# Kernel optimization log

Hardware: AMD Instinct MI355X
Metric: run time of the kernel (lower is better)

## Reference

```python
import jax, jax.numpy as jnp
import numpy as np

DT = 1e-3  # integration timestep (init kwarg dt)


def setup_inputs() -> dict:
    key = jax.random.key(0)
    ks = jax.random.split(key, 10)
    B, T, S, H = 4096, 2048, 1, 64
    # physically sensible signals: v ~ N(0,1), 0 < F_c < F_s so g > 0
    v = jax.random.normal(ks[0], (B, T, S), dtype=jnp.float32)
    F_c = 0.5 + jax.random.uniform(ks[1], (B, T, S), dtype=jnp.float32)
    F_s = F_c + 0.5 + 0.5 * jax.random.uniform(ks[2], (B, T, S), dtype=jnp.float32)
    x = jnp.concatenate([v, F_c, F_s], axis=-1)  # [B, T, 3*S]
    u01 = lambda k, shp: jax.random.uniform(k, shp, minval=0.0, maxval=0.1, dtype=jnp.float32)
    return {
        "x": x,
        "sigma_1": u01(ks[3], (1, S)),
        "sigma_2": u01(ks[4], (1, S)),
        "alpha": u01(ks[5], (1, S)),
        "v_s": u01(ks[6], (1, S)),
        "W1": jax.random.normal(ks[7], (2 * S, H), dtype=jnp.float32) * 0.1,
        "b1": jnp.zeros((H,), jnp.float32),
        "W2": jax.random.normal(ks[8], (H, S), dtype=jnp.float32) * 0.1,
        "b2": jnp.zeros((S,), jnp.float32),
    }


def reference(x, sigma_1, sigma_2, alpha, v_s, W1, b1, W2, b2):
    """LuGreCell.callv3 unrolled over time via lax.scan. x: [B,T,3S] -> F: [B,T,S]."""
    s1 = jnp.abs(sigma_1)
    s2 = jnp.abs(sigma_2)

    def step(sz0, xt):  # sz0: [B,S], xt: [B,3S]
        v, F_c, F_s = jnp.split(xt, 3, axis=-1)
        # sigma_call: MLP on concat([v, sz_0])
        mi = jnp.concatenate([v, sz0], axis=-1)  # [B, 2S]
        sigma_0 = jax.nn.softplus(jnp.tanh(mi @ W1 + b1) @ W2 + b2)  # [B, S]
        g = F_c + (F_s - F_c) * jnp.exp(-jnp.abs(v / v_s) ** alpha)
        k = g * jnp.sign(v)
        sz = k + (sz0 - k) * jnp.exp(-DT * sigma_0 * jnp.abs(v) / g)
        zdot = v - sz * jnp.abs(v) / g  # uses pre-clip sz, as in original
        sz = jnp.clip(sz, -F_s, F_s)
        F = sz + s1 * zdot + s2 * v
        return sz, F

    B = x.shape[0]
    S = x.shape[-1] // 3
    xT = jnp.swapaxes(x, 0, 1)  # [T, B, 3S]
    sz_init = jnp.zeros((B, S), x.dtype)
    _, F_seq = jax.lax.scan(step, sz_init, xT)  # F_seq: [T, B, S]
    return jnp.swapaxes(F_seq, 0, 1)  # [B, T, S]
```

## Files before the change

### kernel.cpp

```cpp
#include <hip/hip_runtime.h>


#define DT 1e-3f
#define NV 256
#define VMINF (-6.6f)
#define VMAXF (6.6f)
#define ZAF   (2.56f)

__global__ __launch_bounds__(320) void coef_kernel(
    const float* __restrict__ W1,
    const float* __restrict__ b1,
    const float* __restrict__ W2,
    const float* __restrict__ b2,
    float4* __restrict__ tabA,
    float*  __restrict__ tabB)
{
    __shared__ float fsh[5];
    const int iv = blockIdx.x;
    const int j  = threadIdx.x >> 6;
    const int h  = threadIdx.x & 63;
    const float v = VMINF + iv * ((VMAXF - VMINF) / (NV - 1));
    const float pn = 0.95105651629f * ZAF;
    const float qn = 0.58778525229f * ZAF;
    const float szv = (j == 0) ? pn : (j == 1) ? -pn
                    : (j == 2) ? qn : (j == 3) ? -qn : 0.f;
    const float pre = fmaf(v, W1[h], fmaf(szv, W1[64 + h], b1[h]));
    float c = W2[h] * tanhf(pre);
#pragma unroll
    for (int o = 32; o; o >>= 1) c += __shfl_down(c, o);
    if (h == 0) {
        const float y = c + b2[0];
        fsh[j] = fmaxf(y, 0.f) + log1pf(expf(-fabsf(y)));
    }
    __syncthreads();
    if (threadIdx.x == 0) {
        const float f0 = fsh[0], f1 = fsh[1], f2 = fsh[2], f3 = fsh[3];
        const float c0 = fsh[4];
        const float P = pn * pn, Q = qn * qn;
        const float ep = 0.5f * (f0 + f1) - c0;
        const float eq = 0.5f * (f2 + f3) - c0;
        const float op = 0.5f * (f0 - f1);
        const float oq = 0.5f * (f2 - f3);
        const float invPQ = 1.f / (P - Q);
        const float c4 = (ep / P - eq / Q) * invPQ;
        const float c2 = ep / P - c4 * P;
        const float c3 = (op / pn - oq / qn) * invPQ;
        const float c1 = op / pn - c3 * P;
        tabA[iv] = make_float4(-DT * c0, -DT * c1, -DT * c2, -DT * c3);
        tabB[iv] = -DT * c4;
    }
}

template <int L>
__device__ __forceinline__ float rb(float v) {
    const int s = __float_as_int(v);
    return __int_as_float(
        __builtin_amdgcn_update_dpp(s, s, 0x150 | L, 0xf, 0xf, false));
}

__global__ __launch_bounds__(256, 1) void lugre_kernel(
    const float* __restrict__ x,
    const float* __restrict__ sigma1,
    const float* __restrict__ sigma2,
    const float* __restrict__ alpha_p,
    const float* __restrict__ vs_p,
    const float4* __restrict__ tabA,
    const float*  __restrict__ tabB,
    float* __restrict__ out,
    int B, int T)
{
    __shared__ float4 sA[NV];
    __shared__ float  sB[NV];

    const int tid = threadIdx.x;
    if (tid < NV) { sA[tid] = tabA[tid]; sB[tid] = tabB[tid]; }

    const int lane16 = tid & 15;
    const int grp    = (tid >> 4) & 3;
    const int w      = tid >> 6;
    const int b      = blockIdx.x * 16 + w * 4 + grp;
    const int NB     = T / 16;

    const float LOG2E = 1.4426950408889634f;
    const float s1v    = fabsf(sigma1[0]);
    const float s2v    = fabsf(sigma2[0]);
    const float s12    = s1v + s2v;
    const float alpha  = alpha_p[0];
    const float inv_vs = 1.0f / vs_p[0];
    const float SVC    = (NV - 1) / (VMAXF - VMINF);
    const float VOFF   = -VMINF * SVC;
    const float IMAX   = 254.999f;

    const float* __restrict__ xb = x + (size_t)b * T * 3;
    float* __restrict__ outb = out + (size_t)b * T;

    auto gather = [&](float v, float4& A0, float4& A1,
                      float& B0, float& B1, float& fr) {
        const float fvr = __builtin_amdgcn_fmed3f(fmaf(v, SVC, VOFF), 0.f, IMAX);
        const float fvf = floorf(fvr);
        fr = fvr - fvf;
        const int iv = (int)fvf;
        A0 = sA[iv]; A1 = sA[iv + 1];
        B0 = sB[iv]; B1 = sB[iv + 1];
    };

    auto finish = [&](float v, float fc, float fs,
                      const float4& A0, const float4& A1,
                      float B0, float B1, float fr,
                      float& e0, float& e1, float& e2, float& e3, float& e4,
                      float& kk, float& ff, float& oQ, float& oSv) {
        const float av = fabsf(v);
        const float u  = av * inv_vs;
        const float lg = __builtin_amdgcn_logf(u);
        const float pw = __builtin_amdgcn_exp2f(alpha * lg);
        const float w_ = __builtin_amdgcn_exp2f(-LOG2E * pw);
        const float g  = fmaf(fs - fc, w_, fc);
        kk = copysignf(g, v);
        const float avg = av * __builtin_amdgcn_rcpf(g);
        e0 = fmaf(fr, A1.x - A0.x, A0.x) * avg;
        e1 = fmaf(fr, A1.y - A0.y, A0.y) * avg;
        e2 = fmaf(fr, A1.z - A0.z, A0.z) * avg;
        e3 = fmaf(fr, A1.w - A0.w, A0.w) * avg;
        e4 = fmaf(fr, B1 - B0, B0) * avg;
        ff = fs;
        oQ  = -(s1v * avg);
        oSv = s12 * v;
    };

    float xcv, xcc, xcf, xnv, xnc, xnf;
    float4 gA0, gA1; float gB0, gB1, gfr;
    float ce0, ce1, ce2, ce3, ce4, ck, cf, cQ, cSv;

    const float* p0 = xb + 3 * lane16;
    const float a0v = p0[0], a0c = p0[1], a0f = p0[2];
    const float* p1 = xb + 48 + 3 * lane16;
    xcv = p1[0]; xcc = p1[1]; xcf = p1[2];
    const float* p2 = xb + 96 + 3 * lane16;
    xnv = p2[0]; xnc = p2[1]; xnf = p2[2];

    __syncthreads();

    {
        float4 aA0, aA1; float aB0, aB1, afr;
        gather(a0v, aA0, aA1, aB0, aB1, afr);
        finish(a0v, a0c, a0f, aA0, aA1, aB0, aB1, afr,
               ce0, ce1, ce2, ce3, ce4, ck, cf, cQ, cSv);
        gather(xcv, gA0, gA1, gB0, gB1, gfr);
    }

    float sz = 0.f;

#define STEP(t) {                                                   \
        const float e0 = rb<t>(ce0), e1 = rb<t>(ce1);               \
        const float e2 = rb<t>(ce2), e3 = rb<t>(ce3);               \
        const float e4 = rb<t>(ce4), kk = rb<t>(ck), ff = rb<t>(cf);\
        const float t1  = fmaf(e1, sz, e0);                         \
        const float t2  = fmaf(e3, sz, e2);                         \
        const float z2  = sz * sz;                                  \
        const float smk = sz - kk;                                  \
        const float t12 = fmaf(t2, z2, t1);                         \
        const float z4  = z2 * z2;                                  \
        const float xd  = fmaf(e4, z4, t12);                        \
        const float u_  = fmaf(xd, 0.5f, 1.f);                      \
        const float w_  = xd * u_;                                  \
        const float szn = fmaf(smk, w_, sz);                        \
        sz = __builtin_amdgcn_fmed3f(szn, -ff, ff);                 \
        kept = (lane16 == t) ? szn : kept; }

#pragma unroll 2
    for (int n = 0; n < NB; ++n) {
        const int bl = (n + 3 < NB) ? n + 3 : NB - 1;
        const float* xp = xb + 48 * bl + 3 * lane16;
        const float lv = xp[0], lc = xp[1], lf = xp[2];

        float4 nA0, nA1; float nB0, nB1, nfr;
        gather(xnv, nA0, nA1, nB0, nB1, nfr);

        float ne0, ne1, ne2, ne3, ne4, nk, nf, nQ, nSv;
        finish(xcv, xcc, xcf, gA0, gA1, gB0, gB1, gfr,
               ne0, ne1, ne2, ne3, ne4, nk, nf, nQ, nSv);

        float kept = 0.f;
        STEP(0);  STEP(1);  STEP(2);  STEP(3);
        STEP(4);  STEP(5);  STEP(6);  STEP(7);
        STEP(8);  STEP(9);  STEP(10); STEP(11);
        STEP(12); STEP(13); STEP(14); STEP(15);

        const float cl = __builtin_amdgcn_fmed3f(kept, -cf, cf);
        outb[16 * n + lane16] = fmaf(cQ, kept, cSv + cl);

        xcv = xnv; xcc = xnc; xcf = xnf;
        xnv = lv;  xnc = lc;  xnf = lf;
        gA0 = nA0; gA1 = nA1; gB0 = nB0; gB1 = nB1; gfr = nfr;
        ce0 = ne0; ce1 = ne1; ce2 = ne2; ce3 = ne3; ce4 = ne4;
        ck = nk; cf = nf; cQ = nQ; cSv = nSv;
    }
#undef STEP
}

extern "C" void kernel_launch(void* const* d_in, const int* in_sizes, int n_in,
                              void* d_out, int out_size, void* d_ws, size_t ws_size,
                              hipStream_t stream) {
    const float* x  = (const float*)d_in[0];
    const float* s1 = (const float*)d_in[1];
    const float* s2 = (const float*)d_in[2];
    const float* al = (const float*)d_in[3];
    const float* vs = (const float*)d_in[4];
    const float* W1 = (const float*)d_in[5];
    const float* b1 = (const float*)d_in[6];
    const float* W2 = (const float*)d_in[7];
    const float* b2 = (const float*)d_in[8];
    float* out = (float*)d_out;

    float4* tabA = (float4*)d_ws;
    float*  tabB = (float*)((char*)d_ws + NV * 16);

    const int T = 2048;
    const int B = out_size / T;

    coef_kernel<<<NV, 320, 0, stream>>>(W1, b1, W2, b2, tabA, tabB);
    lugre_kernel<<<B / 16, 256, 0, stream>>>(x, s1, s2, al, vs, tabA, tabB,
                                             out, B, T);
}
```

Before: 248.8 us.

## Interleave two batch rows per 16-lane group to hide recurrence latency

Each 16-lane group now advances two independent batch rows' sequential recurrences together, interleaving their dependency chains. Blocks shrink to a single 64-thread wave handling eight rows, and the grid is B/8. This trades fewer resident waves and higher register pressure for more instruction-level parallelism within each wave on the latency-bound serial scan.

```diff
diff --git a/kernel.cpp b/kernel.cpp
--- a/kernel.cpp
+++ b/kernel.cpp
@@ -58,7 +58,7 @@
         __builtin_amdgcn_update_dpp(s, s, 0x150 | L, 0xf, 0xf, false));
 }
 
-__global__ __launch_bounds__(256, 1) void lugre_kernel(
+__global__ __launch_bounds__(64, 1) void lugre_kernel(
     const float* __restrict__ x,
     const float* __restrict__ sigma1,
     const float* __restrict__ sigma2,
@@ -73,12 +73,11 @@
     __shared__ float  sB[NV];
 
     const int tid = threadIdx.x;
-    if (tid < NV) { sA[tid] = tabA[tid]; sB[tid] = tabB[tid]; }
+    for (int i = tid; i < NV; i += 64) { sA[i] = tabA[i]; sB[i] = tabB[i]; }
 
     const int lane16 = tid & 15;
-    const int grp    = (tid >> 4) & 3;
-    const int w      = tid >> 6;
-    const int b      = blockIdx.x * 16 + w * 4 + grp;
+    const int grp    = tid >> 4;
+    const int sa     = blockIdx.x * 8 + grp * 2;
     const int NB     = T / 16;
 
     const float LOG2E = 1.4426950408889634f;
@@ -91,8 +90,10 @@
     const float VOFF   = -VMINF * SVC;
     const float IMAX   = 254.999f;
 
-    const float* __restrict__ xb = x + (size_t)b * T * 3;
-    float* __restrict__ outb = out + (size_t)b * T;
+    const float* __restrict__ pA = x + (size_t)sa * T * 3;
+    const float* __restrict__ pB = pA + (size_t)T * 3;
+    float* __restrict__ outA = out + (size_t)sa * T;
+    float* __restrict__ outB = outA + T;
 
     auto gather = [&](float v, float4& A0, float4& A1,
                       float& B0, float& B1, float& fr) {
@@ -127,75 +128,104 @@
         oSv = s12 * v;
     };
 
-    float xcv, xcc, xcf, xnv, xnc, xnf;
-    float4 gA0, gA1; float gB0, gB1, gfr;
-    float ce0, ce1, ce2, ce3, ce4, ck, cf, cQ, cSv;
-
-    const float* p0 = xb + 3 * lane16;
-    const float a0v = p0[0], a0c = p0[1], a0f = p0[2];
-    const float* p1 = xb + 48 + 3 * lane16;
-    xcv = p1[0]; xcc = p1[1]; xcf = p1[2];
-    const float* p2 = xb + 96 + 3 * lane16;
-    xnv = p2[0]; xnc = p2[1]; xnf = p2[2];
+    float a1v, a1c, a1f, a2v, a2c, a2f;
+    float b1v, b1c, b1f, b2v, b2c, b2f;
+    float4 gaA0, gaA1, gbA0, gbA1; float gaB0, gaB1, gafr, gbB0, gbB1, gbfr;
+    float cae0, cae1, cae2, cae3, cae4, cak, caf, caQ, caSv;
+    float cbe0, cbe1, cbe2, cbe3, cbe4, cbk, cbf, cbQ, cbSv;
+
+    const int o0 = 3 * lane16;
+    const float a0v = pA[o0], a0c = pA[o0 + 1], a0f = pA[o0 + 2];
+    const float b0v = pB[o0], b0c = pB[o0 + 1], b0f = pB[o0 + 2];
+    a1v = pA[48 + o0]; a1c = pA[48 + o0 + 1]; a1f = pA[48 + o0 + 2];
+    b1v = pB[48 + o0]; b1c = pB[48 + o0 + 1]; b1f = pB[48 + o0 + 2];
+    a2v = pA[96 + o0]; a2c = pA[96 + o0 + 1]; a2f = pA[96 + o0 + 2];
+    b2v = pB[96 + o0]; b2c = pB[96 + o0 + 1]; b2f = pB[96 + o0 + 2];
 
     __syncthreads();
 
     {
-        float4 aA0, aA1; float aB0, aB1, afr;
-        gather(a0v, aA0, aA1, aB0, aB1, afr);
-        finish(a0v, a0c, a0f, aA0, aA1, aB0, aB1, afr,
-               ce0, ce1, ce2, ce3, ce4, ck, cf, cQ, cSv);
-        gather(xcv, gA0, gA1, gB0, gB1, gfr);
-    }
-
-    float sz = 0.f;
+        float4 tA0, tA1; float tB0, tB1, tfr;
+        gather(a0v, tA0, tA1, tB0, tB1, tfr);
+        finish(a0v, a0c, a0f, tA0, tA1, tB0, tB1, tfr,
+               cae0, cae1, cae2, cae3, cae4, cak, caf, caQ, caSv);
+        gather(b0v, tA0, tA1, tB0, tB1, tfr);
+        finish(b0v, b0c, b0f, tA0, tA1, tB0, tB1, tfr,
+               cbe0, cbe1, cbe2, cbe3, cbe4, cbk, cbf, cbQ, cbSv);
+        gather(a1v, gaA0, gaA1, gaB0, gaB1, gafr);
+        gather(b1v, gbA0, gbA1, gbB0, gbB1, gbfr);
+    }
+
+    float sza = 0.f, szb = 0.f;
+
+#define CH(sz, e0, e1, e2, e3, e4, kk, ff, szn)                     \
+        const float t1##szn = fmaf(e1, sz, e0);                     \
+        const float t2##szn = fmaf(e3, sz, e2);                     \
+        const float z2##szn = sz * sz;                              \
+        const float sk##szn = sz - kk;                              \
+        const float tt##szn = fmaf(t2##szn, z2##szn, t1##szn);      \
+        const float z4##szn = z2##szn * z2##szn;                    \
+        const float xd##szn = fmaf(e4, z4##szn, tt##szn);           \
+        const float uu##szn = fmaf(xd##szn, 0.5f, 1.f);             \
+        const float ww##szn = xd##szn * uu##szn;                    \
+        const float szn     = fmaf(sk##szn, ww##szn, sz);           \
+        sz = __builtin_amdgcn_fmed3f(szn, -ff, ff);
 
 #define STEP(t) {                                                   \
-        const float e0 = rb<t>(ce0), e1 = rb<t>(ce1);               \
-        const float e2 = rb<t>(ce2), e3 = rb<t>(ce3);               \
-        const float e4 = rb<t>(ce4), kk = rb<t>(ck), ff = rb<t>(cf);\
-        const float t1  = fmaf(e1, sz, e0);                         \
-        const float t2  = fmaf(e3, sz, e2);                         \
-        const float z2  = sz * sz;                                  \
-        const float smk = sz - kk;                                  \
-        const float t12 = fmaf(t2, z2, t1);                         \
-        const float z4  = z2 * z2;                                  \
-        const float xd  = fmaf(e4, z4, t12);                        \
-        const float u_  = fmaf(xd, 0.5f, 1.f);                      \
-        const float w_  = xd * u_;                                  \
-        const float szn = fmaf(smk, w_, sz);                        \
-        sz = __builtin_amdgcn_fmed3f(szn, -ff, ff);                 \
-        kept = (lane16 == t) ? szn : kept; }
+        const float ae0 = rb<t>(cae0), ae1 = rb<t>(cae1);           \
+        const float ae2 = rb<t>(cae2), ae3 = rb<t>(cae3);           \
+        const float ae4 = rb<t>(cae4), akk = rb<t>(cak);            \
+        const float aff = rb<t>(caf);                               \
+        const float be0 = rb<t>(cbe0), be1 = rb<t>(cbe1);           \
+        const float be2 = rb<t>(cbe2), be3 = rb<t>(cbe3);           \
+        const float be4 = rb<t>(cbe4), bkk = rb<t>(cbk);            \
+        const float bff = rb<t>(cbf);                               \
+        CH(sza, ae0, ae1, ae2, ae3, ae4, akk, aff, szna##t)         \
+        CH(szb, be0, be1, be2, be3, be4, bkk, bff, sznb##t)         \
+        kepta = (lane16 == t) ? szna##t : kepta;                    \
+        keptb = (lane16 == t) ? sznb##t : keptb; }
 
 #pragma unroll 2
     for (int n = 0; n < NB; ++n) {
         const int bl = (n + 3 < NB) ? n + 3 : NB - 1;
-        const float* xp = xb + 48 * bl + 3 * lane16;
-        const float lv = xp[0], lc = xp[1], lf = xp[2];
-
-        float4 nA0, nA1; float nB0, nB1, nfr;
-        gather(xnv, nA0, nA1, nB0, nB1, nfr);
-
-        float ne0, ne1, ne2, ne3, ne4, nk, nf, nQ, nSv;
-        finish(xcv, xcc, xcf, gA0, gA1, gB0, gB1, gfr,
-               ne0, ne1, ne2, ne3, ne4, nk, nf, nQ, nSv);
-
-        float kept = 0.f;
+        const int ox = 48 * bl + o0;
+        const float lav = pA[ox], lac = pA[ox + 1], laf = pA[ox + 2];
+        const float lbv = pB[ox], lbc = pB[ox + 1], lbf = pB[ox + 2];
+
+        float4 naA0, naA1, nbA0, nbA1;
+        float  naB0, naB1, nafr, nbB0, nbB1, nbfr;
+        gather(a2v, naA0, naA1, naB0, naB1, nafr);
+        gather(b2v, nbA0, nbA1, nbB0, nbB1, nbfr);
+
+        float nae0, nae1, nae2, nae3, nae4, nak, naf, naQ, naSv;
+        float nbe0, nbe1, nbe2, nbe3, nbe4, nbk, nbf, nbQ, nbSv;
+        finish(a1v, a1c, a1f, gaA0, gaA1, gaB0, gaB1, gafr,
+               nae0, nae1, nae2, nae3, nae4, nak, naf, naQ, naSv);
+        finish(b1v, b1c, b1f, gbA0, gbA1, gbB0, gbB1, gbfr,
+               nbe0, nbe1, nbe2, nbe3, nbe4, nbk, nbf, nbQ, nbSv);
+
+        float kepta = 0.f, keptb = 0.f;
         STEP(0);  STEP(1);  STEP(2);  STEP(3);
         STEP(4);  STEP(5);  STEP(6);  STEP(7);
         STEP(8);  STEP(9);  STEP(10); STEP(11);
         STEP(12); STEP(13); STEP(14); STEP(15);
 
-        const float cl = __builtin_amdgcn_fmed3f(kept, -cf, cf);
-        outb[16 * n + lane16] = fmaf(cQ, kept, cSv + cl);
-
-        xcv = xnv; xcc = xnc; xcf = xnf;
-        xnv = lv;  xnc = lc;  xnf = lf;
-        gA0 = nA0; gA1 = nA1; gB0 = nB0; gB1 = nB1; gfr = nfr;
-        ce0 = ne0; ce1 = ne1; ce2 = ne2; ce3 = ne3; ce4 = ne4;
-        ck = nk; cf = nf; cQ = nQ; cSv = nSv;
+        const float acl = __builtin_amdgcn_fmed3f(kepta, -caf, caf);
+        outA[16 * n + lane16] = fmaf(caQ, kepta, caSv + acl);
+        const float bcl = __builtin_amdgcn_fmed3f(keptb, -cbf, cbf);
+        outB[16 * n + lane16] = fmaf(cbQ, keptb, cbSv + bcl);
+
+        a1v = a2v; a1c = a2c; a1f = a2f;  a2v = lav; a2c = lac; a2f = laf;
+        b1v = b2v; b1c = b2c; b1f = b2f;  b2v = lbv; b2c = lbc; b2f = lbf;
+        gaA0 = naA0; gaA1 = naA1; gaB0 = naB0; gaB1 = naB1; gafr = nafr;
+        gbA0 = nbA0; gbA1 = nbA1; gbB0 = nbB0; gbB1 = nbB1; gbfr = nbfr;
+        cae0 = nae0; cae1 = nae1; cae2 = nae2; cae3 = nae3; cae4 = nae4;
+        cak = nak; caf = naf; caQ = naQ; caSv = naSv;
+        cbe0 = nbe0; cbe1 = nbe1; cbe2 = nbe2; cbe3 = nbe3; cbe4 = nbe4;
+        cbk = nbk; cbf = nbf; cbQ = nbQ; cbSv = nbSv;
     }
 #undef STEP
+#undef CH
 }
 
 extern "C" void kernel_launch(void* const* d_in, const int* in_sizes, int n_in,
@@ -219,6 +249,6 @@
     const int B = out_size / T;
 
     coef_kernel<<<NV, 320, 0, stream>>>(W1, b1, W2, b2, tabA, tabB);
-    lugre_kernel<<<B / 16, 256, 0, stream>>>(x, s1, s2, al, vs, tabA, tabB,
-                                             out, B, T);
-}
+    lugre_kernel<<<B / 8, 64, 0, stream>>>(x, s1, s2, al, vs, tabA, tabB,
+                                           out, B, T);
+}
```

Result: slower. 356.5 us (+43.3%).
